# Optimization experiments

Hardware: AMD Instinct MI355X
Metric: run time of the kernel (lower is better)

Reference implementation:

```python
import jax, jax.numpy as jnp
import numpy as np
import math

DIM_IN = 512
DIM_OUT = 512
KERNEL = 3
STYLE_DIM = 2 * 128
LIN_SCALE = 1.0 / math.sqrt(STYLE_DIM)      # EqualLinear scale (lr_mul=1)
CONV_SCALE = 1.0 / math.sqrt(DIM_IN * KERNEL ** 2)  # fan_in = dim_in * k**2 (as in source)
PAD = KERNEL // 2


def setup_inputs() -> dict:
    key = jax.random.key(0)
    ks = jax.random.split(key, 5)
    B, T = 16, 2048
    x = jax.random.normal(ks[0], (B, DIM_IN, T), dtype=jnp.float32)
    c_src = jax.random.normal(ks[1], (B, 128), dtype=jnp.float32)
    c_trg = jax.random.normal(ks[2], (B, 128), dtype=jnp.float32)
    style_w = jax.random.normal(ks[3], (DIM_IN, STYLE_DIM), dtype=jnp.float32)
    style_b = jnp.ones((DIM_IN,), dtype=jnp.float32)  # bias_init=1
    weight = jax.random.normal(ks[4], (1, DIM_OUT, DIM_IN, KERNEL), dtype=jnp.float32)
    return {"x": x, "c_src": c_src, "c_trg": c_trg,
            "style_w": style_w, "style_b": style_b, "weight": weight}


def reference(x, c_src, c_trg, style_w, style_b, weight):
    B = x.shape[0]
    # EqualLinear: style code s [B, dim_in]
    c = jnp.concatenate([c_src, c_trg], axis=-1)              # [B, 256]
    s = c @ (style_w * LIN_SCALE).T + style_b                 # [B, dim_in]
    # Modulate: w [B, dim_out, dim_in, k]
    w = CONV_SCALE * weight * s[:, None, :, None]
    # Demodulate over (dim_in, k)
    demod = jax.lax.rsqrt(jnp.sum(w * w, axis=(2, 3)) + 1e-8)  # [B, dim_out]
    w = w * demod[:, :, None, None]
    # Per-sample conv1d, padding 'same' (pad = k//2), vmapped over batch
    def conv1(xi, wi):
        # xi: [dim_in, T], wi: [dim_out, dim_in, k]
        out = jax.lax.conv_general_dilated(
            xi[None], wi, window_strides=(1,), padding=[(PAD, PAD)],
            dimension_numbers=("NCH", "OIH", "NCH"))
        return out[0]                                          # [dim_out, T]
    return jax.vmap(conv1)(x, w)                               # [B, dim_out, T]
```

## Files before the change

kernel.cpp:

```cpp
#include <hip/hip_runtime.h>
#include <cstdint>
#include <cstddef>


#define LIN_SCALE  0.0625f
#define CONV_SCALE 0.014731391f

#define B_   16
#define CIN  512
#define COUT 512
#define T_   2048
#define TP   2050

typedef __bf16 bf16x8 __attribute__((ext_vector_type(8)));
typedef float  f32x4  __attribute__((ext_vector_type(4)));
typedef unsigned short u16x8 __attribute__((ext_vector_type(8)));
typedef unsigned short u16x2 __attribute__((ext_vector_type(2)));

#define AS1 __attribute__((address_space(1)))
#define AS3 __attribute__((address_space(3)))

__device__ inline unsigned short f2bf(float f) {
  __bf16 h = (__bf16)f;
  return __builtin_bit_cast(unsigned short, h);
}

__global__ __launch_bounds__(256) void style_kernel(const float* __restrict__ c_src,
                                                    const float* __restrict__ c_trg,
                                                    const float* __restrict__ sw,
                                                    const float* __restrict__ sb,
                                                    float* __restrict__ s) {
  __shared__ float c[256];
  const int b = blockIdx.y;
  const int tid = threadIdx.x;
  c[tid] = (tid < 128) ? c_src[b * 128 + tid] : c_trg[b * 128 + tid - 128];
  __syncthreads();
  const int w = tid >> 6, lane = tid & 63;
  #pragma unroll
  for (int rr = 0; rr < 16; ++rr) {
    const int i = blockIdx.x * 64 + w * 16 + rr;
    const float* row = sw + (size_t)i * 256;
    float acc = row[lane] * c[lane] + row[lane + 64] * c[lane + 64]
              + row[lane + 128] * c[lane + 128] + row[lane + 192] * c[lane + 192];
    #pragma unroll
    for (int off = 32; off; off >>= 1) acc += __shfl_down(acc, off, 64);
    if (lane == 0) s[b * 512 + i] = acc * LIN_SCALE + sb[i];
  }
}

__global__ __launch_bounds__(256) void modw_kernel(const float* __restrict__ weight,
                                                   const float* __restrict__ s,
                                                   unsigned short* __restrict__ Wm) {
  const int o = blockIdx.x;
  const int tid = threadIdx.x;
  __shared__ float wsh[1536];
  __shared__ float svs[16 * 512];
  __shared__ float partial[16][4];
  __shared__ float demv[16];

  #pragma unroll
  for (int j = tid; j < 1536; j += 256) wsh[j] = weight[(size_t)o * 1536 + j];
  #pragma unroll
  for (int j = tid; j < 16 * 512; j += 256) svs[j] = s[j];
  __syncthreads();

  float wr[6];
  #pragma unroll
  for (int q = 0; q < 6; ++q) wr[q] = wsh[tid * 6 + q] * CONV_SCALE;

  const int lane = tid & 63, w = tid >> 6;
  float ssb[16];
  #pragma unroll
  for (int b = 0; b < 16; ++b) {
    const float s0 = svs[b * 512 + 2 * tid];
    const float s1 = svs[b * 512 + 2 * tid + 1];
    float ss = 0.f;
    #pragma unroll
    for (int q = 0; q < 3; ++q) { float v = wr[q] * s0; ss += v * v; }
    #pragma unroll
    for (int q = 3; q < 6; ++q) { float v = wr[q] * s1; ss += v * v; }
    ssb[b] = ss;
  }
  #pragma unroll
  for (int b = 0; b < 16; ++b) {
    float ss = ssb[b];
    #pragma unroll
    for (int off = 32; off; off >>= 1) ss += __shfl_down(ss, off, 64);
    if (lane == 0) partial[b][w] = ss;
  }
  __syncthreads();
  if (tid < 16)
    demv[tid] = rsqrtf(partial[tid][0] + partial[tid][1] + partial[tid][2] + partial[tid][3] + 1e-8f);
  __syncthreads();

  #pragma unroll
  for (int b = 0; b < 16; ++b) {
    const float dem = demv[b];
    const float s0 = svs[b * 512 + 2 * tid] * dem;
    const float s1 = svs[b * 512 + 2 * tid + 1] * dem;
    #pragma unroll
    for (int k = 0; k < 3; ++k) {
      u16x2 v;
      v.x = f2bf(wr[k] * s0);
      v.y = f2bf(wr[3 + k] * s1);
      *(u16x2*)&Wm[(((size_t)b * 3 + k) * 512 + o) * 512 + 2 * tid] = v;
    }
  }
}

__global__ __launch_bounds__(256) void transpose_kernel(const float* __restrict__ x,
                                                        unsigned short* __restrict__ xT) {
  __shared__ float tile[64][65];
  const int b = blockIdx.z, i0 = blockIdx.y * 64, t0 = blockIdx.x * 64;
  const int tid = threadIdx.x;

  const int lr = tid >> 4;
  const int lc = (tid & 15) * 4;
  const float* xb = x + ((size_t)b * CIN + i0) * T_ + t0;
  #pragma unroll
  for (int p = 0; p < 4; ++p) {
    const int r = p * 16 + lr;
    const float4 v = *(const float4*)(xb + (size_t)r * T_ + lc);
    tile[r][lc + 0] = v.x; tile[r][lc + 1] = v.y;
    tile[r][lc + 2] = v.z; tile[r][lc + 3] = v.w;
  }
  if (blockIdx.x == 0 && tid < 8)
    *(u16x8*)&xT[(size_t)b * TP * CIN + i0 + tid * 8] = (u16x8){0,0,0,0,0,0,0,0};
  if (blockIdx.x == gridDim.x - 1 && tid < 8)
    *(u16x8*)&xT[((size_t)b * TP + TP - 1) * CIN + i0 + tid * 8] = (u16x8){0,0,0,0,0,0,0,0};
  __syncthreads();

  const int st = tid >> 3;
  const int si = (tid & 7) * 8;
  unsigned short* xTb = xT + ((size_t)b * TP + 1 + t0) * CIN + i0;
  #pragma unroll
  for (int p = 0; p < 2; ++p) {
    const int t = p * 32 + st;
    u16x8 v;
    #pragma unroll
    for (int q = 0; q < 8; ++q) v[q] = f2bf(tile[si + q][t]);
    *(u16x8*)&xTb[(size_t)t * CIN + si] = v;
  }
}

#define BM 128
#define BN 256
#define BK 32

__global__ __launch_bounds__(256, 2) void gemm_kernel(const unsigned short* __restrict__ Wm,
                                                      const unsigned short* __restrict__ xT,
                                                      float* __restrict__ out) {
  __shared__ unsigned short lA[3 * 128 * 32];
  __shared__ unsigned short lB[258 * 32];

  const int id  = blockIdx.x;
  const int xcd = id & 7;
  const int j   = id >> 3;
  const int b   = xcd + 8 * (j >> 5);
  const int r   = j & 31;
  const int o0  = (r >> 3) * BM;
  const int t0  = (r & 7) * BN;

  const int tid  = threadIdx.x;
  const int lane = tid & 63;
  const int wm   = ((tid >> 6) & 1) * 64;
  const int wn   = (tid >> 7) * 128;
  const int rl   = lane & 15;
  const int kc   = lane >> 4;

  const unsigned short* gW = Wm + ((size_t)b * 3 * 512 + o0) * 512;
  const unsigned short* gX = xT + ((size_t)b * TP + t0) * CIN;

  f32x4 acc[4][8];
  #pragma unroll
  for (int i = 0; i < 4; ++i)
    #pragma unroll
    for (int jj = 0; jj < 8; ++jj) acc[i][jj] = (f32x4){0.f, 0.f, 0.f, 0.f};

  for (int kk = 0; kk < 16; ++kk) {
    const int i0 = kk * 32;
    __syncthreads();
    #pragma unroll
    for (int q = 0; q < 6; ++q) {
      const int ci  = q * 256 + tid;
      const int row = ci >> 2;
      const int tap = row >> 7;
      const int ar  = row & 127;
      const int gc  = ((ci & 3) ^ ((ar >> 1) & 3)) * 8;
      __builtin_amdgcn_global_load_lds(
          (const AS1 void*)(gW + (size_t)tap * 262144 + (size_t)ar * 512 + i0 + gc),
          (AS3 void*)(&lA[ci * 8]), 16, 0, 0);
    }
    #pragma unroll
    for (int q = 0; q < 4; ++q) {
      const int ci  = q * 256 + tid;
      const int row = ci >> 2;
      const int gc  = ((ci & 3) ^ ((row >> 1) & 3)) * 8;
      __builtin_amdgcn_global_load_lds(
          (const AS1 void*)(gX + (size_t)row * CIN + i0 + gc),
          (AS3 void*)(&lB[ci * 8]), 16, 0, 0);
    }
    if (tid < 8) {
      const int ci  = 1024 + tid;
      const int row = ci >> 2;
      const int gc  = ((ci & 3) ^ ((row >> 1) & 3)) * 8;
      __builtin_amdgcn_global_load_lds(
          (const AS1 void*)(gX + (size_t)row * CIN + i0 + gc),
          (AS3 void*)(&lB[ci * 8]), 16, 0, 0);
    }
    __syncthreads();

    #pragma unroll
    for (int tap = 0; tap < 3; ++tap) {
      bf16x8 af[4], bfr[8];
      #pragma unroll
      for (int mi = 0; mi < 4; ++mi) {
        const int ra = wm + mi * 16 + rl;
        af[mi] = *(const bf16x8*)&lA[((tap * 128 + ra) * 4 + (kc ^ ((ra >> 1) & 3))) * 8];
      }
      #pragma unroll
      for (int ni = 0; ni < 8; ++ni) {
        const int rb = wn + ni * 16 + rl + tap;
        bfr[ni] = *(const bf16x8*)&lB[(rb * 4 + (kc ^ ((rb >> 1) & 3))) * 8];
      }
      #pragma unroll
      for (int mi = 0; mi < 4; ++mi)
        #pragma unroll
        for (int ni = 0; ni < 8; ++ni)
          acc[mi][ni] = __builtin_amdgcn_mfma_f32_16x16x32_bf16(af[mi], bfr[ni], acc[mi][ni], 0, 0, 0);
    }
  }

  float* ob = out + ((size_t)b * COUT + o0 + wm) * T_ + t0 + wn;
  const int rrow = (lane >> 4) * 4;
  const int ccol = lane & 15;
  #pragma unroll
  for (int mi = 0; mi < 4; ++mi)
    #pragma unroll
    for (int ni = 0; ni < 8; ++ni)
      #pragma unroll
      for (int rr = 0; rr < 4; ++rr)
        ob[(size_t)(mi * 16 + rrow + rr) * T_ + ni * 16 + ccol] = acc[mi][ni][rr];
}

extern "C" void kernel_launch(void* const* d_in, const int* in_sizes, int n_in,
                              void* d_out, int out_size, void* d_ws, size_t ws_size,
                              hipStream_t stream) {
  const float* x       = (const float*)d_in[0];
  const float* c_src   = (const float*)d_in[1];
  const float* c_trg   = (const float*)d_in[2];
  const float* style_w = (const float*)d_in[3];
  const float* style_b = (const float*)d_in[4];
  const float* weight  = (const float*)d_in[5];
  float* out = (float*)d_out;

  char* ws = (char*)d_ws;
  float* s_buf          = (float*)ws;
  unsigned short* Wm    = (unsigned short*)(ws + 32768);
  unsigned short* xTbuf = (unsigned short*)(ws + 32768 + 25165824);

  style_kernel<<<dim3(8, 16), 256, 0, stream>>>(c_src, c_trg, style_w, style_b, s_buf);
  modw_kernel<<<dim3(COUT), 256, 0, stream>>>(weight, s_buf, Wm);
  transpose_kernel<<<dim3(T_ / 64, CIN / 64, B_), 256, 0, stream>>>(x, xTbuf);
  gemm_kernel<<<dim3(512), 256, 0, stream>>>(Wm, xTbuf, out);
}
```

Before: 190.3 us.

## Factor style modulation into input and demodulation into epilogue, share one weight

Rather than building a per-batch modulated bf16 weight tensor (16×3×512×512), the style scale is applied to x during the transpose, and the demodulation factor is applied per output row in the GEMM epilogue. The GEMM then reads a single shared bf16 weight for all batches. This removes a large weight-materialisation write and its re-reads, and improves cache reuse of the weight. In exchange, rounding changes because s is folded into the bf16 input, and the epilogue does an extra multiply.

```diff
diff --git a/kernel.cpp b/kernel.cpp
--- a/kernel.cpp
+++ b/kernel.cpp
@@ -48,25 +48,35 @@
   }
 }
 
-__global__ __launch_bounds__(256) void modw_kernel(const float* __restrict__ weight,
-                                                   const float* __restrict__ s,
-                                                   unsigned short* __restrict__ Wm) {
+__global__ __launch_bounds__(256) void demod_kernel(const float* __restrict__ weight,
+                                                    const float* __restrict__ s,
+                                                    float* __restrict__ demod,
+                                                    unsigned short* __restrict__ Wb) {
   const int o = blockIdx.x;
   const int tid = threadIdx.x;
   __shared__ float wsh[1536];
   __shared__ float svs[16 * 512];
   __shared__ float partial[16][4];
-  __shared__ float demv[16];
-
-  #pragma unroll
-  for (int j = tid; j < 1536; j += 256) wsh[j] = weight[(size_t)o * 1536 + j];
-  #pragma unroll
-  for (int j = tid; j < 16 * 512; j += 256) svs[j] = s[j];
+
+  #pragma unroll
+  for (int j = tid; j < 384; j += 256)
+    ((float4*)wsh)[j] = ((const float4*)(weight + (size_t)o * 1536))[j];
+  #pragma unroll
+  for (int j = tid; j < 2048; j += 256)
+    ((float4*)svs)[j] = ((const float4*)s)[j];
   __syncthreads();
 
   float wr[6];
   #pragma unroll
   for (int q = 0; q < 6; ++q) wr[q] = wsh[tid * 6 + q] * CONV_SCALE;
+
+  #pragma unroll
+  for (int k = 0; k < 3; ++k) {
+    u16x2 v;
+    v.x = f2bf(wr[k]);
+    v.y = f2bf(wr[3 + k]);
+    *(u16x2*)&Wb[((size_t)(k * 512 + o)) * 512 + 2 * tid] = v;
+  }
 
   const int lane = tid & 63, w = tid >> 6;
   float ssb[16];
@@ -90,29 +100,19 @@
   }
   __syncthreads();
   if (tid < 16)
-    demv[tid] = rsqrtf(partial[tid][0] + partial[tid][1] + partial[tid][2] + partial[tid][3] + 1e-8f);
-  __syncthreads();
-
-  #pragma unroll
-  for (int b = 0; b < 16; ++b) {
-    const float dem = demv[b];
-    const float s0 = svs[b * 512 + 2 * tid] * dem;
-    const float s1 = svs[b * 512 + 2 * tid + 1] * dem;
-    #pragma unroll
-    for (int k = 0; k < 3; ++k) {
-      u16x2 v;
-      v.x = f2bf(wr[k] * s0);
-      v.y = f2bf(wr[3 + k] * s1);
-      *(u16x2*)&Wm[(((size_t)b * 3 + k) * 512 + o) * 512 + 2 * tid] = v;
-    }
-  }
+    demod[(size_t)tid * 512 + o] =
+        rsqrtf(partial[tid][0] + partial[tid][1] + partial[tid][2] + partial[tid][3] + 1e-8f);
 }
 
 __global__ __launch_bounds__(256) void transpose_kernel(const float* __restrict__ x,
+                                                        const float* __restrict__ s,
                                                         unsigned short* __restrict__ xT) {
   __shared__ float tile[64][65];
+  __shared__ float ss[64];
   const int b = blockIdx.z, i0 = blockIdx.y * 64, t0 = blockIdx.x * 64;
   const int tid = threadIdx.x;
+
+  if (tid < 64) ss[tid] = s[(size_t)b * 512 + i0 + tid];
 
   const int lr = tid >> 4;
   const int lc = (tid & 15) * 4;
@@ -132,13 +132,16 @@
 
   const int st = tid >> 3;
   const int si = (tid & 7) * 8;
+  float sv[8];
+  #pragma unroll
+  for (int q = 0; q < 8; ++q) sv[q] = ss[si + q];
   unsigned short* xTb = xT + ((size_t)b * TP + 1 + t0) * CIN + i0;
   #pragma unroll
   for (int p = 0; p < 2; ++p) {
     const int t = p * 32 + st;
     u16x8 v;
     #pragma unroll
-    for (int q = 0; q < 8; ++q) v[q] = f2bf(tile[si + q][t]);
+    for (int q = 0; q < 8; ++q) v[q] = f2bf(tile[si + q][t] * sv[q]);
     *(u16x8*)&xTb[(size_t)t * CIN + si] = v;
   }
 }
@@ -147,8 +150,9 @@
 #define BN 256
 #define BK 32
 
-__global__ __launch_bounds__(256, 2) void gemm_kernel(const unsigned short* __restrict__ Wm,
+__global__ __launch_bounds__(256, 2) void gemm_kernel(const unsigned short* __restrict__ Wb,
                                                       const unsigned short* __restrict__ xT,
+                                                      const float* __restrict__ demod,
                                                       float* __restrict__ out) {
   __shared__ unsigned short lA[3 * 128 * 32];
   __shared__ unsigned short lB[258 * 32];
@@ -168,7 +172,7 @@
   const int rl   = lane & 15;
   const int kc   = lane >> 4;
 
-  const unsigned short* gW = Wm + ((size_t)b * 3 * 512 + o0) * 512;
+  const unsigned short* gW = Wb + (size_t)o0 * 512;
   const unsigned short* gX = xT + ((size_t)b * TP + t0) * CIN;
 
   f32x4 acc[4][8];
@@ -232,15 +236,20 @@
   }
 
   float* ob = out + ((size_t)b * COUT + o0 + wm) * T_ + t0 + wn;
+  const float* dm = demod + (size_t)b * 512 + o0 + wm;
   const int rrow = (lane >> 4) * 4;
   const int ccol = lane & 15;
   #pragma unroll
-  for (int mi = 0; mi < 4; ++mi)
+  for (int mi = 0; mi < 4; ++mi) {
+    float dr[4];
+    #pragma unroll
+    for (int rr = 0; rr < 4; ++rr) dr[rr] = dm[mi * 16 + rrow + rr];
     #pragma unroll
     for (int ni = 0; ni < 8; ++ni)
       #pragma unroll
       for (int rr = 0; rr < 4; ++rr)
-        ob[(size_t)(mi * 16 + rrow + rr) * T_ + ni * 16 + ccol] = acc[mi][ni][rr];
+        ob[(size_t)(mi * 16 + rrow + rr) * T_ + ni * 16 + ccol] = acc[mi][ni][rr] * dr[rr];
+  }
 }
 
 extern "C" void kernel_launch(void* const* d_in, const int* in_sizes, int n_in,
@@ -256,11 +265,12 @@
 
   char* ws = (char*)d_ws;
   float* s_buf          = (float*)ws;
-  unsigned short* Wm    = (unsigned short*)(ws + 32768);
-  unsigned short* xTbuf = (unsigned short*)(ws + 32768 + 25165824);
+  float* demod_buf      = (float*)(ws + 32768);
+  unsigned short* Wb    = (unsigned short*)(ws + 65536);
+  unsigned short* xTbuf = (unsigned short*)(ws + 65536 + 1572864);
 
   style_kernel<<<dim3(8, 16), 256, 0, stream>>>(c_src, c_trg, style_w, style_b, s_buf);
-  modw_kernel<<<dim3(COUT), 256, 0, stream>>>(weight, s_buf, Wm);
-  transpose_kernel<<<dim3(T_ / 64, CIN / 64, B_), 256, 0, stream>>>(x, xTbuf);
-  gemm_kernel<<<dim3(512), 256, 0, stream>>>(Wm, xTbuf, out);
-}
+  demod_kernel<<<dim3(COUT), 256, 0, stream>>>(weight, s_buf, demod_buf, Wb);
+  transpose_kernel<<<dim3(T_ / 64, CIN / 64, B_), 256, 0, stream>>>(x, s_buf, xTbuf);
+  gemm_kernel<<<dim3(512), 256, 0, stream>>>(Wb, xTbuf, demod_buf, out);
+}
```

Result: faster. 181.3 us (-4.8%).
